# Kernel optimization log

Hardware: AMD Instinct MI355X
Metric: run time of the kernel (lower is better)

## Reference

```python
import jax, jax.numpy as jnp
import numpy as np

EPS = 1e-6

def _phi(u):
    # positive feature map used by linear attention
    return jax.nn.elu(u) + 1.0

def setup_inputs() -> dict:
    key = jax.random.key(0)
    ks = jax.random.split(key, 5)
    B, T, D = 8, 2048, 512  # batch, seq_len, d_model == in_features == out_features
    scale = 1.0 / np.sqrt(D)
    x = jax.random.normal(ks[0], (B, T, D), dtype=jnp.float32)
    Wq = (jax.random.normal(ks[1], (D, D), dtype=jnp.float32) * scale)
    Wk = (jax.random.normal(ks[2], (D, D), dtype=jnp.float32) * scale)
    Wv = (jax.random.normal(ks[3], (D, D), dtype=jnp.float32) * scale)
    Wp = (jax.random.normal(ks[4], (D, D), dtype=jnp.float32) * scale)  # output projection (bias=False)
    return {"x": x, "Wq": Wq, "Wk": Wk, "Wv": Wv, "Wp": Wp}

def reference(x, Wq, Wk, Wv, Wp):
    # x: [B, T, D]
    B, T, D = x.shape
    q = _phi(x @ Wq)  # [B, T, D]
    k = _phi(x @ Wk)  # [B, T, D]
    v = x @ Wv        # [B, T, D]

    # recurrent linear-attention cell, stepped over time via lax.scan
    def step(carry, qkv):
        S, z = carry              # S: [B, D, D] running sum of k^T v; z: [B, D] running sum of k
        qt, kt, vt = qkv          # each [B, D]
        S = S + kt[:, :, None] * vt[:, None, :]
        z = z + kt
        num = jnp.einsum('bd,bde->be', qt, S)        # [B, D]
        den = jnp.einsum('bd,bd->b', qt, z) + EPS    # [B]
        return (S, z), num / den[:, None]

    qT = jnp.swapaxes(q, 0, 1)  # [T, B, D]
    kT = jnp.swapaxes(k, 0, 1)
    vT = jnp.swapaxes(v, 0, 1)
    init = (jnp.zeros((B, D, D), dtype=x.dtype), jnp.zeros((B, D), dtype=x.dtype))
    _, yT = jax.lax.scan(step, init, (qT, kT, vT))  # yT: [T, B, D]
    y = jnp.swapaxes(yT, 0, 1)                      # [B, T, D]
    return y @ Wp                                   # final bias-free projection
```

## Files before the change

### kernel.cpp

```cpp
#include <hip/hip_runtime.h>


typedef __attribute__((ext_vector_type(4))) float f32x4;
typedef __attribute__((ext_vector_type(8))) __bf16 bf16x8;
typedef __attribute__((ext_vector_type(8))) unsigned short ushort8;

constexpr size_t OFF_XB  = 0;
constexpr size_t OFF_WT  = OFF_XB + 16777216;
constexpr size_t OFF_Q   = OFF_WT + 2097152;
constexpr size_t OFF_KK  = OFF_Q  + 16777216;
constexpr size_t OFF_KT  = OFF_KK + 16777216;
constexpr size_t OFF_VT  = OFF_KT + 16777216;
constexpr size_t OFF_MT  = OFF_VT + 16777216;
constexpr size_t OFF_Y   = OFF_MT + 33554432;
constexpr size_t OFF_ZP  = OFF_Y  + 16777216;
constexpr size_t WS_NEED = OFF_ZP + 262144;

__device__ __forceinline__ unsigned short bfbits(float f) {
  __bf16 h = (__bf16)f;
  return __builtin_bit_cast(unsigned short, h);
}
__device__ __forceinline__ float bff(unsigned short u) {
  return (float)__builtin_bit_cast(__bf16, u);
}

__device__ __forceinline__ void gload16(const void* g, void* l) {
  __builtin_amdgcn_global_load_lds((const __attribute__((address_space(1))) void*)g,
                                   (__attribute__((address_space(3))) void*)l, 16, 0, 0);
}

__device__ __forceinline__ void stage_half(const char* gRow0, size_t ld2, int k0b,
                                           char* ldsHalf, int w, int lane) {
#pragma unroll
  for (int i = 0; i < 2; ++i) {
    int L = (w << 10) + (lane << 4) + (i << 13);
    int r = L >> 7;
    int cb = (L & 127) ^ ((r & 7) << 4);
    gload16(gRow0 + (size_t)r * ld2 + k0b + cb, ldsHalf + (w << 10) + (i << 13));
  }
}

__device__ __forceinline__ void stage_q64(const char* gRow0, size_t ld2, int k0b,
                                          char* lds, int tid) {
  int L = tid << 4;
  int r = L >> 7;
  int cb = (L & 127) ^ ((r & 7) << 4);
  gload16(gRow0 + (size_t)r * ld2 + k0b + cb, lds + L);
}

__device__ __forceinline__ const bf16x8* frag_at(const char* halfBase, int rowInHalf,
                                                 int colByte) {
  int lin = (rowInHalf << 7) + colByte;
  lin ^= (rowInHalf & 7) << 4;
  return (const bf16x8*)(halfBase + lin);
}

#define QUADH(mh, nh)                                                                  \
  _Pragma("unroll") for (int mm = 0; mm < 2; ++mm)                                     \
  _Pragma("unroll") for (int nn = 0; nn < 2; ++nn)                                     \
  _Pragma("unroll") for (int s = 0; s < 2; ++s)                                        \
      acc[(mh)*2 + mm][(nh)*2 + nn] = __builtin_amdgcn_mfma_f32_16x16x32_bf16(         \
          af[(mh)*2 + mm][s], bg[(nh)*2 + nn][s], acc[(mh)*2 + mm][(nh)*2 + nn], 0, 0, 0);

#define PHASE_TAILH(MH, NH)                                      \
  __builtin_amdgcn_s_barrier();                                  \
  asm volatile("s_waitcnt lgkmcnt(0)" ::: "memory");             \
  __builtin_amdgcn_sched_barrier(0);                             \
  __builtin_amdgcn_s_setprio(1);                                 \
  QUADH(MH, NH);                                                 \
  __builtin_amdgcn_s_setprio(0);                                 \
  __builtin_amdgcn_s_barrier();

__device__ __forceinline__ void core8h(const char* Ab, size_t lda2, const char* Bb,
                                       size_t ldb2, int nt, char* sA, char* sB,
                                       f32x4 (&acc)[4][4], int w, int lane) {
  const int wr = w >> 2, wc = w & 3;
  const int fr = lane & 15, foB = (lane >> 4) << 4;
  const int brow = (wc & 1) << 6;
  const char* gB1 = Bb + (size_t)128 * ldb2;
  bf16x8 af[4][2], bg[4][2];

  stage_half(Ab, lda2, 0, sA + 0, w, lane);
  stage_half(Bb, ldb2, 0, sB + 0, w, lane);
  stage_half(gB1, ldb2, 0, sB + 16384, w, lane);
  if (nt > 1) {
    stage_half(Ab, lda2, 128, sA + 16384, w, lane);
    asm volatile("s_waitcnt vmcnt(2)" ::: "memory");
  } else {
    asm volatile("s_waitcnt vmcnt(0)" ::: "memory");
  }
  __builtin_amdgcn_sched_barrier(0);
  __builtin_amdgcn_s_barrier();

  for (int t = 0; t < nt; ++t) {
    const int buf = t & 1;
    const char* cA = sA + buf * 16384;
    const char* cB = sB + buf * 32768 + (wc >> 1) * 16384;
    char* nA = sA + buf * 16384;
    char* nB = sB + (buf ^ 1) * 32768;
    const int kb1 = (t + 1) << 7, kb2 = (t + 2) << 7;
    const bool stB = (t + 1 < nt), stA = (t + 2 < nt);

#pragma unroll
    for (int m = 0; m < 2; ++m)
#pragma unroll
      for (int s = 0; s < 2; ++s)
        af[m][s] = *frag_at(cA, wr * 64 + m * 16 + fr, s * 64 + foB);
#pragma unroll
    for (int n = 0; n < 2; ++n)
#pragma unroll
      for (int s = 0; s < 2; ++s)
        bg[n][s] = *frag_at(cB, brow + n * 16 + fr, s * 64 + foB);
    if (stB) stage_half(Bb, ldb2, kb1, nB + 0, w, lane);
    PHASE_TAILH(0, 0)

#pragma unroll
    for (int m = 2; m < 4; ++m)
#pragma unroll
      for (int s = 0; s < 2; ++s)
        af[m][s] = *frag_at(cA, wr * 64 + m * 16 + fr, s * 64 + foB);
    if (stB) stage_half(gB1, ldb2, kb1, nB + 16384, w, lane);
    PHASE_TAILH(1, 0)

#pragma unroll
    for (int n = 2; n < 4; ++n)
#pragma unroll
      for (int s = 0; s < 2; ++s)
        bg[n][s] = *frag_at(cB, brow + n * 16 + fr, s * 64 + foB);
    if (stA) stage_half(Ab, lda2, kb2, nA, w, lane);
    PHASE_TAILH(0, 1)

    if (t < nt - 1) {
      if (stA) {
        asm volatile("s_waitcnt vmcnt(2)" ::: "memory");
      } else {
        asm volatile("s_waitcnt vmcnt(0)" ::: "memory");
      }
      __builtin_amdgcn_sched_barrier(0);
    }
    PHASE_TAILH(1, 1)
  }
}

__device__ __forceinline__ void core8h_ldsA(const char* sG, const char* Bb, size_t ldb2,
                                            int nt, char* sB, f32x4 (&acc)[4][4],
                                            int w, int lane) {
  const int wr = w >> 2, wc = w & 3;
  const int fr = lane & 15, foB = (lane >> 4) << 4;
  const int brow = (wc & 1) << 6;
  const char* gB1 = Bb + (size_t)128 * ldb2;
  bf16x8 af[4][2], bg[4][2];

  stage_half(Bb, ldb2, 0, sB + 0, w, lane);
  stage_half(gB1, ldb2, 0, sB + 16384, w, lane);
  asm volatile("s_waitcnt vmcnt(0)" ::: "memory");
  __builtin_amdgcn_sched_barrier(0);
  __builtin_amdgcn_s_barrier();

  for (int t = 0; t < nt; ++t) {
    const int buf = t & 1;
    const char* cA = sG + t * 16384;
    const char* cB = sB + buf * 32768 + (wc >> 1) * 16384;
    char* nB = sB + (buf ^ 1) * 32768;
    if (t + 1 < nt) {
      stage_half(Bb, ldb2, (t + 1) << 7, nB + 0, w, lane);
      stage_half(gB1, ldb2, (t + 1) << 7, nB + 16384, w, lane);
    }
#pragma unroll
    for (int m = 0; m < 4; ++m)
#pragma unroll
      for (int s = 0; s < 2; ++s)
        af[m][s] = *frag_at(cA, wr * 64 + m * 16 + fr, s * 64 + foB);
#pragma unroll
    for (int n = 0; n < 4; ++n)
#pragma unroll
      for (int s = 0; s < 2; ++s)
        bg[n][s] = *frag_at(cB, brow + n * 16 + fr, s * 64 + foB);
    __builtin_amdgcn_s_setprio(1);
#pragma unroll
    for (int m = 0; m < 4; ++m)
#pragma unroll
      for (int n = 0; n < 4; ++n)
#pragma unroll
        for (int s = 0; s < 2; ++s)
          acc[m][n] = __builtin_amdgcn_mfma_f32_16x16x32_bf16(af[m][s], bg[n][s],
                                                              acc[m][n], 0, 0, 0);
    __builtin_amdgcn_s_setprio(0);
    if (t + 1 < nt) {
      asm volatile("s_waitcnt vmcnt(0)" ::: "memory");
      __builtin_amdgcn_sched_barrier(0);
      __builtin_amdgcn_s_barrier();
    }
  }
}

#define ACC4_INIT                                    \
  f32x4 acc[4][4];                                   \
  _Pragma("unroll") for (int m_ = 0; m_ < 4; ++m_)   \
  _Pragma("unroll") for (int n_ = 0; n_ < 4; ++n_)   \
      acc[m_][n_] = f32x4{0.f, 0.f, 0.f, 0.f};

#define ACC4_ZERO                                    \
  _Pragma("unroll") for (int m_ = 0; m_ < 4; ++m_)   \
  _Pragma("unroll") for (int n_ = 0; n_ < 4; ++n_)   \
      acc[m_][n_] = f32x4{0.f, 0.f, 0.f, 0.f};

__global__ __launch_bounds__(512, 2) void k8_qkvt(const ushort* __restrict__ xb,
                                                  const ushort* __restrict__ wt,
                                                  ushort* __restrict__ qb,
                                                  ushort* __restrict__ kkb,
                                                  ushort* __restrict__ Kt,
                                                  ushort* __restrict__ Vt,
                                                  float* __restrict__ zsumH) {
  extern __shared__ char smem[];
  const int o = blockIdx.x;
  const int wg = (o & 7) * 64 + (o >> 3);
  const int mt = wg >> 2, ct = wg & 3;
  const int tid = threadIdx.x, w = tid >> 6, lane = tid & 63;
  const int wr = w >> 2, wc = w & 3;
  const int fr = lane & 15, foB = (lane >> 4) << 4, q4 = (lane >> 4) << 2;
  const char* Ab = (const char*)(xb + (size_t)mt * 128 * 512);
  const char* Bz[3];
  Bz[0] = (const char*)(wt + (size_t)ct * 65536);
  Bz[1] = (const char*)(wt + 262144 + (size_t)ct * 65536);
  Bz[2] = (const char*)(wt + 524288 + (size_t)ct * 65536);
  char* sA = smem;
  char* sB0 = smem + 32768;
  char* sB1 = smem + 65536;
  char* sB2 = smem + 98304;

  f32x4 acc[3][4][2];
#pragma unroll
  for (int z = 0; z < 3; ++z)
#pragma unroll
    for (int m = 0; m < 4; ++m)
#pragma unroll
      for (int n = 0; n < 2; ++n) acc[z][m][n] = f32x4{0.f, 0.f, 0.f, 0.f};

  stage_half(Ab, 1024, 0, sA, w, lane);
  stage_half(Bz[0], 1024, 0, sB0, w, lane);
  stage_half(Bz[1], 1024, 0, sB1, w, lane);
  stage_half(Bz[2], 1024, 0, sB2, w, lane);
  asm volatile("s_waitcnt vmcnt(0)" ::: "memory");
  __builtin_amdgcn_sched_barrier(0);
  __builtin_amdgcn_s_barrier();

  for (int t = 0; t < 8; ++t) {
    const int buf = t & 1;
    const int bo = buf << 14, nbo = (buf ^ 1) << 14;
    if (t + 1 < 8) {
      const int kb = (t + 1) << 7;
      stage_half(Ab, 1024, kb, sA + nbo, w, lane);
      stage_half(Bz[0], 1024, kb, sB0 + nbo, w, lane);
      stage_half(Bz[1], 1024, kb, sB1 + nbo, w, lane);
      stage_half(Bz[2], 1024, kb, sB2 + nbo, w, lane);
    }
    bf16x8 af[4][2], bg[3][2][2];
#pragma unroll
    for (int m = 0; m < 4; ++m)
#pragma unroll
      for (int s = 0; s < 2; ++s)
        af[m][s] = *frag_at(sA + bo, wr * 64 + m * 16 + fr, s * 64 + foB);
#pragma unroll
    for (int z = 0; z < 3; ++z)
#pragma unroll
      for (int n = 0; n < 2; ++n)
#pragma unroll
        for (int s = 0; s < 2; ++s)
          bg[z][n][s] = *frag_at((z == 0 ? sB0 : z == 1 ? sB1 : sB2) + bo,
                                 wc * 32 + n * 16 + fr, s * 64 + foB);
    __builtin_amdgcn_s_setprio(1);
#pragma unroll
    for (int z = 0; z < 3; ++z)
#pragma unroll
      for (int m = 0; m < 4; ++m)
#pragma unroll
        for (int n = 0; n < 2; ++n)
#pragma unroll
          for (int s = 0; s < 2; ++s)
            acc[z][m][n] = __builtin_amdgcn_mfma_f32_16x16x32_bf16(af[m][s], bg[z][n][s],
                                                                   acc[z][m][n], 0, 0, 0);
    __builtin_amdgcn_s_setprio(0);
    if (t + 1 < 8) {
      asm volatile("s_waitcnt vmcnt(0)" ::: "memory");
    }
    __builtin_amdgcn_sched_barrier(0);
    __builtin_amdgcn_s_barrier();
  }

  const size_t row0 = (size_t)mt * 128 + wr * 64;
  const size_t col0 = (size_t)ct * 128 + wc * 32;
#pragma unroll
  for (int m = 0; m < 4; ++m)
#pragma unroll
    for (int n = 0; n < 2; ++n)
#pragma unroll
      for (int r = 0; r < 4; ++r) {
        float v = acc[0][m][n][r];
        v = v > 0.f ? v + 1.f : __expf(v);
        qb[(row0 + m * 16 + q4 + r) * 512 + col0 + n * 16 + fr] = bfbits(v);
      }
#pragma unroll
  for (int m = 0; m < 4; ++m)
#pragma unroll
    for (int n = 0; n < 2; ++n) {
      ushort4 ov;
      ov.x = bfbits(acc[2][m][n][0]);
      ov.y = bfbits(acc[2][m][n][1]);
      ov.z = bfbits(acc[2][m][n][2]);
      ov.w = bfbits(acc[2][m][n][3]);
      *(ushort4*)&Vt[(col0 + n * 16 + fr) * 16384 + row0 + m * 16 + q4] = ov;
    }
  float zs[2] = {0.f, 0.f};
#pragma unroll
  for (int m = 0; m < 4; ++m)
#pragma unroll
    for (int n = 0; n < 2; ++n) {
      float ph[4];
#pragma unroll
      for (int r = 0; r < 4; ++r) {
        float v = acc[1][m][n][r];
        ph[r] = v > 0.f ? v + 1.f : __expf(v);
        kkb[(row0 + m * 16 + q4 + r) * 512 + col0 + n * 16 + fr] = bfbits(ph[r]);
        zs[n] += ph[r];
      }
      ushort4 ov;
      ov.x = bfbits(ph[0]); ov.y = bfbits(ph[1]); ov.z = bfbits(ph[2]); ov.w = bfbits(ph[3]);
      *(ushort4*)&Kt[(col0 + n * 16 + fr) * 16384 + row0 + m * 16 + q4] = ov;
    }
#pragma unroll
  for (int n = 0; n < 2; ++n) {
    zs[n] += __shfl_xor(zs[n], 16, 64);
    zs[n] += __shfl_xor(zs[n], 32, 64);
  }
  float* zbuf = (float*)smem;
  if (lane < 16) {
#pragma unroll
    for (int n = 0; n < 2; ++n) zbuf[wr * 128 + wc * 32 + n * 16 + fr] = zs[n];
  }
  __syncthreads();
  if (tid < 128)
    zsumH[(size_t)mt * 512 + ct * 128 + tid] = zbuf[tid] + zbuf[128 + tid];
}

__global__ __launch_bounds__(512, 2) void k8_mtst(const ushort* __restrict__ Kt,
                                                  const ushort* __restrict__ Vt,
                                                  ushort* __restrict__ Mt) {
  __shared__ __align__(16) char smem[49152];
  const int o = blockIdx.x;
  const int b = o & 7, r8 = o >> 3;
  const int et = r8 >> 3, dt = r8 & 7;
  const int tid = threadIdx.x, w = tid >> 6, lane = tid & 63;
  const int wr = w >> 2, wc = w & 3, fr = lane & 15;
  const int foB = (lane >> 4) << 4, q4 = (lane >> 4) << 2;
  const char* Ab = (const char*)(Vt + (size_t)et * 128 * 16384 + b * 2048);
  const char* Bb = (const char*)(Kt + (size_t)dt * 64 * 16384 + b * 2048);
  f32x4 acc[4];
#pragma unroll
  for (int m = 0; m < 4; ++m) acc[m] = f32x4{0.f, 0.f, 0.f, 0.f};

  stage_half(Ab, 32768, 0, smem, w, lane);
  stage_q64(Bb, 32768, 0, smem + 32768, tid);
  asm volatile("s_waitcnt vmcnt(0)" ::: "memory");
  __builtin_amdgcn_sched_barrier(0);
  __builtin_amdgcn_s_barrier();

  const int colg = dt * 64 + wc * 16 + fr;
  for (int kk = 0; kk < 32; ++kk) {
    const int c = kk >> 2, buf = kk & 1;
    if ((kk & 3) == 0) {
      ushort* Sc = Mt + (size_t)(b * 8 + c) * 262144 + colg;
#pragma unroll
      for (int m = 0; m < 4; ++m)
#pragma unroll
        for (int r = 0; r < 4; ++r)
          Sc[(size_t)(et * 128 + wr * 64 + m * 16 + q4 + r) * 512] = bfbits(acc[m][r]);
    }
    if (kk + 1 < 32) {
      const int k0b = ((kk + 1) >> 2) * 512 + ((kk + 1) & 3) * 128;
      stage_half(Ab, 32768, k0b, smem + ((buf ^ 1) << 14), w, lane);
      stage_q64(Bb, 32768, k0b, smem + 32768 + ((buf ^ 1) << 13), tid);
    }
    const char* cA = smem + (buf << 14);
    const char* cB = smem + 32768 + (buf << 13);
    bf16x8 af[4][2], bg[2];
#pragma unroll
    for (int s = 0; s < 2; ++s) bg[s] = *frag_at(cB, wc * 16 + fr, s * 64 + foB);
#pragma unroll
    for (int m = 0; m < 4; ++m)
#pragma unroll
      for (int s = 0; s < 2; ++s)
        af[m][s] = *frag_at(cA, wr * 64 + m * 16 + fr, s * 64 + foB);
    __builtin_amdgcn_s_setprio(1);
#pragma unroll
    for (int m = 0; m < 4; ++m)
#pragma unroll
      for (int s = 0; s < 2; ++s)
        acc[m] = __builtin_amdgcn_mfma_f32_16x16x32_bf16(af[m][s], bg[s], acc[m], 0, 0, 0);
    __builtin_amdgcn_s_setprio(0);
    asm volatile("s_waitcnt vmcnt(0)" ::: "memory");
    __builtin_amdgcn_sched_barrier(0);
    __builtin_amdgcn_s_barrier();
  }
}

__global__ __launch_bounds__(512, 2) void k8_y(const ushort* __restrict__ qb,
                                               const ushort* __restrict__ kkb,
                                               const ushort* __restrict__ St,
                                               const ushort* __restrict__ Vt,
                                               const float* __restrict__ zsumH,
                                               ushort* __restrict__ Y) {
  extern __shared__ char smem[];
  const int o = blockIdx.x;
  const int wg = (o & 7) * 32 + (o >> 3);
  const int bc = wg >> 2, rh = (wg >> 1) & 1, ch = wg & 1;
  const int b = bc >> 3, c = bc & 7;
  const int tid = threadIdx.x, w = tid >> 6, lane = tid & 63;
  const int wr = w >> 2, wc = w & 3, fr = lane & 15, q4 = (lane >> 4) << 2;
  char* sA = smem + 65536;
  char* sB = smem + 98304;
  const char* qptr = (const char*)(qb + (size_t)bc * 131072 + (size_t)rh * 65536);

  ACC4_INIT
  core8h(qptr, 1024, (const char*)(kkb + (size_t)bc * 131072), 1024, 8, sA, sB, acc, w, lane);

  float rs[4][4];
#pragma unroll
  for (int m = 0; m < 4; ++m)
#pragma unroll
    for (int r = 0; r < 4; ++r) rs[m][r] = 0.f;
#pragma unroll
  for (int m = 0; m < 4; ++m)
#pragma unroll
    for (int n = 0; n < 4; ++n)
#pragma unroll
      for (int r = 0; r < 4; ++r) {
        int rowL = wr * 64 + m * 16 + q4 + r;
        int col = wc * 64 + n * 16 + fr;
        float v = (col <= rh * 128 + rowL) ? acc[m][n][r] : 0.f;
        rs[m][r] += v;
        int byte = (rowL << 7) + ((col & 63) << 1);
        byte ^= (rowL & 7) << 4;
        *(__bf16*)(smem + (wc << 14) + byte) = (__bf16)v;
      }
#pragma unroll
  for (int m = 0; m < 4; ++m)
#pragma unroll
    for (int r = 0; r < 4; ++r) {
      rs[m][r] += __shfl_xor(rs[m][r], 1, 64);
      rs[m][r] += __shfl_xor(rs[m][r], 2, 64);
      rs[m][r] += __shfl_xor(rs[m][r], 4, 64);
      rs[m][r] += __shfl_xor(rs[m][r], 8, 64);
    }
  float* red = (float*)sA;
  float* zpl = red + 512;
  float* dend = zpl + 512;
  if (fr == 0) {
#pragma unroll
    for (int m = 0; m < 4; ++m)
#pragma unroll
      for (int r = 0; r < 4; ++r) red[wc * 128 + wr * 64 + m * 16 + q4 + r] = rs[m][r];
  }
  {
    float a = 0.f;
    for (int cp = 0; cp < c; ++cp)
      a += zsumH[(size_t)((b * 8 + cp) * 2) * 512 + tid] +
           zsumH[(size_t)((b * 8 + cp) * 2 + 1) * 512 + tid];
    zpl[tid] = a;
  }
  __syncthreads();
  {
    int rl = tid >> 2, quarter = tid & 3;
    int trow = bc * 256 + rh * 128 + rl;
    const ushort* qrow = qb + (size_t)trow * 512 + quarter * 128;
    const float* zq = zpl + quarter * 128;
    float s = 0.f;
    for (int j = 0; j < 128; j += 8) {
      ushort8 qv = *(const ushort8*)&qrow[j];
#pragma unroll
      for (int u = 0; u < 8; ++u) s = fmaf(bff(qv[u]), zq[j + u], s);
    }
    s += __shfl_xor(s, 1, 64);
    s += __shfl_xor(s, 2, 64);
    if (quarter == 0)
      dend[rl] = s + red[rl] + red[128 + rl] + red[256 + rl] + red[384 + rl] + 1e-6f;
  }
  __syncthreads();
  float dinv[4][4];
#pragma unroll
  for (int m = 0; m < 4; ++m)
#pragma unroll
    for (int r = 0; r < 4; ++r) dinv[m][r] = 1.f / dend[wr * 64 + m * 16 + q4 + r];
  __syncthreads();

  ACC4_ZERO
  core8h(qptr, 1024, (const char*)(St + (size_t)bc * 262144 + (size_t)ch * 131072), 1024, 8,
         sA, sB, acc, w, lane);
  core8h_ldsA(smem, (const char*)(Vt + (size_t)ch * 256 * 16384 + (size_t)bc * 256), 32768,
              rh ? 4 : 2, sB, acc, w, lane);

#pragma unroll
  for (int m = 0; m < 4; ++m)
#pragma unroll
    for (int n = 0; n < 4; ++n)
#pragma unroll
      for (int r = 0; r < 4; ++r) {
        size_t row = (size_t)bc * 256 + rh * 128 + wr * 64 + m * 16 + q4 + r;
        size_t col = (size_t)ch * 256 + wc * 64 + n * 16 + fr;
        Y[row * 512 + col] = bfbits(acc[m][n][r] * dinv[m][r]);
      }
}

__global__ __launch_bounds__(512, 2) void k8_out(const ushort* __restrict__ Y,
                                                 const ushort* __restrict__ wt,
                                                 float* __restrict__ out) {
  extern __shared__ char smem[];
  const int o = blockIdx.x;
  const int wg = (o & 7) * 32 + (o >> 3);
  const int mt = wg >> 1, ct = wg & 1;
  const int tid = threadIdx.x, w = tid >> 6, lane = tid & 63;
  ACC4_INIT
  core8h((const char*)(Y + (size_t)mt * 65536), 1024,
         (const char*)(wt + 786432 + (size_t)ct * 131072), 1024, 8,
         smem, smem + 32768, acc, w, lane);
  const int wr = w >> 2, wc = w & 3, fr = lane & 15, q4 = (lane >> 4) << 2;
  const size_t row0 = (size_t)mt * 128 + wr * 64;
  const size_t col0 = (size_t)ct * 256 + wc * 64;
#pragma unroll
  for (int m = 0; m < 4; ++m)
#pragma unroll
    for (int n = 0; n < 4; ++n)
#pragma unroll
      for (int r = 0; r < 4; ++r)
        out[(row0 + m * 16 + q4 + r) * 512 + col0 + n * 16 + fr] = acc[m][n][r];
}

__global__ __launch_bounds__(256) void k_pre(const float* __restrict__ x,
                                             const float* __restrict__ Wq,
                                             const float* __restrict__ Wk,
                                             const float* __restrict__ Wv,
                                             const float* __restrict__ Wp,
                                             ushort* __restrict__ xb,
                                             ushort* __restrict__ wt) {
  __shared__ float tile[64][65];
  if (blockIdx.x < 4096) {
    size_t i = ((size_t)blockIdx.x * 256 + threadIdx.x) * 8;
    float4 f0 = *(const float4*)&x[i], f1 = *(const float4*)&x[i + 4];
    ushort8 ov;
    ov[0] = bfbits(f0.x); ov[1] = bfbits(f0.y); ov[2] = bfbits(f0.z); ov[3] = bfbits(f0.w);
    ov[4] = bfbits(f1.x); ov[5] = bfbits(f1.y); ov[6] = bfbits(f1.z); ov[7] = bfbits(f1.w);
    *(ushort8*)&xb[i] = ov;
  } else {
    const int g = blockIdx.x - 4096;
    const int bz = g >> 6, rem = g & 63, bxw = rem >> 3, byw = rem & 7;
    const float* src = bz == 0 ? Wq : bz == 1 ? Wk : bz == 2 ? Wv : Wp;
    ushort* dst = wt + (size_t)bz * 262144;
    const int d0 = bxw * 64, n0 = byw * 64;
    const int tr = threadIdx.x >> 4, tc = (threadIdx.x & 15) << 2;
#pragma unroll
    for (int it = 0; it < 4; ++it) {
      float4 f = *(const float4*)&src[(size_t)(d0 + it * 16 + tr) * 512 + n0 + tc];
      tile[it * 16 + tr][tc + 0] = f.x;
      tile[it * 16 + tr][tc + 1] = f.y;
      tile[it * 16 + tr][tc + 2] = f.z;
      tile[it * 16 + tr][tc + 3] = f.w;
    }
    __syncthreads();
#pragma unroll
    for (int it = 0; it < 4; ++it) {
      int n = it * 16 + tr;
      ushort4 ov;
      ov.x = bfbits(tile[tc + 0][n]);
      ov.y = bfbits(tile[tc + 1][n]);
      ov.z = bfbits(tile[tc + 2][n]);
      ov.w = bfbits(tile[tc + 3][n]);
      *(ushort4*)&dst[(size_t)(n0 + n) * 512 + d0 + tc] = ov;
    }
  }
}

extern "C" void kernel_launch(void* const* d_in, const int* in_sizes, int n_in,
                              void* d_out, int out_size, void* d_ws, size_t ws_size,
                              hipStream_t stream) {
  const float* x  = (const float*)d_in[0];
  const float* Wq = (const float*)d_in[1];
  const float* Wk = (const float*)d_in[2];
  const float* Wv = (const float*)d_in[3];
  const float* Wp = (const float*)d_in[4];
  float* out = (float*)d_out;
  char* ws8 = (char*)d_ws;
  if (ws_size < WS_NEED) return;

  ushort* xb  = (ushort*)(ws8 + OFF_XB);
  ushort* wt  = (ushort*)(ws8 + OFF_WT);
  ushort* qb  = (ushort*)(ws8 + OFF_Q);
  ushort* kkb = (ushort*)(ws8 + OFF_KK);
  ushort* Kt  = (ushort*)(ws8 + OFF_KT);
  ushort* Vt  = (ushort*)(ws8 + OFF_VT);
  ushort* Mt  = (ushort*)(ws8 + OFF_MT);
  ushort* Y   = (ushort*)(ws8 + OFF_Y);
  float*  zpH = (float*)(ws8 + OFF_ZP);

  constexpr int SMEM_QKVT = 131072, SMEM_H = 98304, SMEM_Y = 163840;
  hipFuncSetAttribute((const void*)k8_qkvt, hipFuncAttributeMaxDynamicSharedMemorySize, SMEM_QKVT);
  hipFuncSetAttribute((const void*)k8_y,    hipFuncAttributeMaxDynamicSharedMemorySize, SMEM_Y);
  hipFuncSetAttribute((const void*)k8_out,  hipFuncAttributeMaxDynamicSharedMemorySize, SMEM_H);

  k_pre<<<4352, 256, 0, stream>>>(x, Wq, Wk, Wv, Wp, xb, wt);
  k8_qkvt<<<512, 512, SMEM_QKVT, stream>>>(xb, wt, qb, kkb, Kt, Vt, zpH);
  k8_mtst<<<256, 512, 0, stream>>>(Kt, Vt, Mt);
  k8_y<<<256, 512, SMEM_Y, stream>>>(qb, kkb, Mt, Vt, zpH, Y);
  k8_out<<<256, 512, SMEM_H, stream>>>(Y, wt, out);
}
```

Before: 127.2 us.

## Move intra-chunk QK^T gram and denominator into the state kernel

The masked intra-chunk score matrix (q·kᵀ), its row sums and the normalizing denominator move out of the output kernel. They are now computed by extra blocks added to the chunk-state kernel, so both pieces of work run concurrently across 384 blocks. The masked scores go to a global bf16 buffer and the denominators to a float buffer. The output kernel then streams the scores from global memory through the generic GEMM core, which cuts its LDS use from 160KB to 96KB and shortens its critical path. The cost is an extra global round trip for the score matrix, about 8MB, plus the extra workspace.

After: 127.6 us. About the same (+0.3%).

```diff
diff --git a/kernel.cpp b/kernel.cpp
--- a/kernel.cpp
+++ b/kernel.cpp
@@ -11,10 +11,12 @@
 constexpr size_t OFF_KK  = OFF_Q  + 16777216;
 constexpr size_t OFF_KT  = OFF_KK + 16777216;
 constexpr size_t OFF_VT  = OFF_KT + 16777216;
-constexpr size_t OFF_MT  = OFF_VT + 16777216;
+constexpr size_t OFF_G   = OFF_VT + 16777216;
+constexpr size_t OFF_MT  = OFF_G  + 8388608;
 constexpr size_t OFF_Y   = OFF_MT + 33554432;
 constexpr size_t OFF_ZP  = OFF_Y  + 16777216;
-constexpr size_t WS_NEED = OFF_ZP + 262144;
+constexpr size_t OFF_DEN = OFF_ZP + 262144;
+constexpr size_t WS_NEED = OFF_DEN + 65536;
 
 __device__ __forceinline__ unsigned short bfbits(float f) {
   __bf16 h = (__bf16)f;
@@ -139,58 +141,6 @@
       __builtin_amdgcn_sched_barrier(0);
     }
     PHASE_TAILH(1, 1)
-  }
-}
-
-__device__ __forceinline__ void core8h_ldsA(const char* sG, const char* Bb, size_t ldb2,
-                                            int nt, char* sB, f32x4 (&acc)[4][4],
-                                            int w, int lane) {
-  const int wr = w >> 2, wc = w & 3;
-  const int fr = lane & 15, foB = (lane >> 4) << 4;
-  const int brow = (wc & 1) << 6;
-  const char* gB1 = Bb + (size_t)128 * ldb2;
-  bf16x8 af[4][2], bg[4][2];
-
-  stage_half(Bb, ldb2, 0, sB + 0, w, lane);
-  stage_half(gB1, ldb2, 0, sB + 16384, w, lane);
-  asm volatile("s_waitcnt vmcnt(0)" ::: "memory");
-  __builtin_amdgcn_sched_barrier(0);
-  __builtin_amdgcn_s_barrier();
-
-  for (int t = 0; t < nt; ++t) {
-    const int buf = t & 1;
-    const char* cA = sG + t * 16384;
-    const char* cB = sB + buf * 32768 + (wc >> 1) * 16384;
-    char* nB = sB + (buf ^ 1) * 32768;
-    if (t + 1 < nt) {
-      stage_half(Bb, ldb2, (t + 1) << 7, nB + 0, w, lane);
-      stage_half(gB1, ldb2, (t + 1) << 7, nB + 16384, w, lane);
-    }
-#pragma unroll
-    for (int m = 0; m < 4; ++m)
-#pragma unroll
-      for (int s = 0; s < 2; ++s)
-        af[m][s] = *frag_at(cA, wr * 64 + m * 16 + fr, s * 64 + foB);
-#pragma unroll
-    for (int n = 0; n < 4; ++n)
-#pragma unroll
-      for (int s = 0; s < 2; ++s)
-        bg[n][s] = *frag_at(cB, brow + n * 16 + fr, s * 64 + foB);
-    __builtin_amdgcn_s_setprio(1);
-#pragma unroll
-    for (int m = 0; m < 4; ++m)
-#pragma unroll
-      for (int n = 0; n < 4; ++n)
-#pragma unroll
-        for (int s = 0; s < 2; ++s)
-          acc[m][n] = __builtin_amdgcn_mfma_f32_16x16x32_bf16(af[m][s], bg[n][s],
-                                                              acc[m][n], 0, 0, 0);
-    __builtin_amdgcn_s_setprio(0);
-    if (t + 1 < nt) {
-      asm volatile("s_waitcnt vmcnt(0)" ::: "memory");
-      __builtin_amdgcn_sched_barrier(0);
-      __builtin_amdgcn_s_barrier();
-    }
   }
 }
 
@@ -343,162 +293,171 @@
     zsumH[(size_t)mt * 512 + ct * 128 + tid] = zbuf[tid] + zbuf[128 + tid];
 }
 
-__global__ __launch_bounds__(512, 2) void k8_mtst(const ushort* __restrict__ Kt,
-                                                  const ushort* __restrict__ Vt,
-                                                  ushort* __restrict__ Mt) {
-  __shared__ __align__(16) char smem[49152];
-  const int o = blockIdx.x;
-  const int b = o & 7, r8 = o >> 3;
-  const int et = r8 >> 3, dt = r8 & 7;
+__global__ __launch_bounds__(512, 2) void k8_mg(const ushort* __restrict__ Kt,
+                                                const ushort* __restrict__ Vt,
+                                                const ushort* __restrict__ qb,
+                                                const ushort* __restrict__ kkb,
+                                                const float* __restrict__ zsumH,
+                                                ushort* __restrict__ Mt,
+                                                ushort* __restrict__ Gg,
+                                                float* __restrict__ den) {
+  extern __shared__ char smem[];
+  const int bx = blockIdx.x;
   const int tid = threadIdx.x, w = tid >> 6, lane = tid & 63;
   const int wr = w >> 2, wc = w & 3, fr = lane & 15;
   const int foB = (lane >> 4) << 4, q4 = (lane >> 4) << 2;
-  const char* Ab = (const char*)(Vt + (size_t)et * 128 * 16384 + b * 2048);
-  const char* Bb = (const char*)(Kt + (size_t)dt * 64 * 16384 + b * 2048);
-  f32x4 acc[4];
-#pragma unroll
-  for (int m = 0; m < 4; ++m) acc[m] = f32x4{0.f, 0.f, 0.f, 0.f};
-
-  stage_half(Ab, 32768, 0, smem, w, lane);
-  stage_q64(Bb, 32768, 0, smem + 32768, tid);
-  asm volatile("s_waitcnt vmcnt(0)" ::: "memory");
-  __builtin_amdgcn_sched_barrier(0);
-  __builtin_amdgcn_s_barrier();
-
-  const int colg = dt * 64 + wc * 16 + fr;
-  for (int kk = 0; kk < 32; ++kk) {
-    const int c = kk >> 2, buf = kk & 1;
-    if ((kk & 3) == 0) {
-      ushort* Sc = Mt + (size_t)(b * 8 + c) * 262144 + colg;
-#pragma unroll
-      for (int m = 0; m < 4; ++m)
-#pragma unroll
-        for (int r = 0; r < 4; ++r)
-          Sc[(size_t)(et * 128 + wr * 64 + m * 16 + q4 + r) * 512] = bfbits(acc[m][r]);
-    }
-    if (kk + 1 < 32) {
-      const int k0b = ((kk + 1) >> 2) * 512 + ((kk + 1) & 3) * 128;
-      stage_half(Ab, 32768, k0b, smem + ((buf ^ 1) << 14), w, lane);
-      stage_q64(Bb, 32768, k0b, smem + 32768 + ((buf ^ 1) << 13), tid);
-    }
-    const char* cA = smem + (buf << 14);
-    const char* cB = smem + 32768 + (buf << 13);
-    bf16x8 af[4][2], bg[2];
-#pragma unroll
-    for (int s = 0; s < 2; ++s) bg[s] = *frag_at(cB, wc * 16 + fr, s * 64 + foB);
-#pragma unroll
-    for (int m = 0; m < 4; ++m)
-#pragma unroll
-      for (int s = 0; s < 2; ++s)
-        af[m][s] = *frag_at(cA, wr * 64 + m * 16 + fr, s * 64 + foB);
-    __builtin_amdgcn_s_setprio(1);
-#pragma unroll
-    for (int m = 0; m < 4; ++m)
-#pragma unroll
-      for (int s = 0; s < 2; ++s)
-        acc[m] = __builtin_amdgcn_mfma_f32_16x16x32_bf16(af[m][s], bg[s], acc[m], 0, 0, 0);
-    __builtin_amdgcn_s_setprio(0);
+  if (bx < 256) {
+    const int b = bx & 7, r8 = bx >> 3;
+    const int et = r8 >> 3, dt = r8 & 7;
+    const char* Ab = (const char*)(Vt + (size_t)et * 128 * 16384 + b * 2048);
+    const char* Bb = (const char*)(Kt + (size_t)dt * 64 * 16384 + b * 2048);
+    f32x4 acc[4];
+#pragma unroll
+    for (int m = 0; m < 4; ++m) acc[m] = f32x4{0.f, 0.f, 0.f, 0.f};
+
+    stage_half(Ab, 32768, 0, smem, w, lane);
+    stage_q64(Bb, 32768, 0, smem + 32768, tid);
     asm volatile("s_waitcnt vmcnt(0)" ::: "memory");
     __builtin_amdgcn_sched_barrier(0);
     __builtin_amdgcn_s_barrier();
+
+    const int colg = dt * 64 + wc * 16 + fr;
+    for (int kk = 0; kk < 32; ++kk) {
+      const int c = kk >> 2, buf = kk & 1;
+      if ((kk & 3) == 0) {
+        ushort* Sc = Mt + (size_t)(b * 8 + c) * 262144 + colg;
+#pragma unroll
+        for (int m = 0; m < 4; ++m)
+#pragma unroll
+          for (int r = 0; r < 4; ++r)
+            Sc[(size_t)(et * 128 + wr * 64 + m * 16 + q4 + r) * 512] = bfbits(acc[m][r]);
+      }
+      if (kk + 1 < 32) {
+        const int k0b = ((kk + 1) >> 2) * 512 + ((kk + 1) & 3) * 128;
+        stage_half(Ab, 32768, k0b, smem + ((buf ^ 1) << 14), w, lane);
+        stage_q64(Bb, 32768, k0b, smem + 32768 + ((buf ^ 1) << 13), tid);
+      }
+      const char* cA = smem + (buf << 14);
+      const char* cB = smem + 32768 + (buf << 13);
+      bf16x8 af[4][2], bg[2];
+#pragma unroll
+      for (int s = 0; s < 2; ++s) bg[s] = *frag_at(cB, wc * 16 + fr, s * 64 + foB);
+#pragma unroll
+      for (int m = 0; m < 4; ++m)
+#pragma unroll
+        for (int s = 0; s < 2; ++s)
+          af[m][s] = *frag_at(cA, wr * 64 + m * 16 + fr, s * 64 + foB);
+      __builtin_amdgcn_s_setprio(1);
+#pragma unroll
+      for (int m = 0; m < 4; ++m)
+#pragma unroll
+        for (int s = 0; s < 2; ++s)
+          acc[m] = __builtin_amdgcn_mfma_f32_16x16x32_bf16(af[m][s], bg[s], acc[m], 0, 0, 0);
+      __builtin_amdgcn_s_setprio(0);
+      asm volatile("s_waitcnt vmcnt(0)" ::: "memory");
+      __builtin_amdgcn_sched_barrier(0);
+      __builtin_amdgcn_s_barrier();
+    }
+  } else {
+    const int g = bx - 256;
+    const int bc = g >> 1, rh = g & 1;
+    const int b = bc >> 3, c = bc & 7;
+    char* sA = smem;
+    char* sB = smem + 32768;
+    ACC4_INIT
+    core8h((const char*)(qb + (size_t)bc * 131072 + (size_t)rh * 65536), 1024,
+           (const char*)(kkb + (size_t)bc * 131072), 1024, 8, sA, sB, acc, w, lane);
+
+    float rs[4][4];
+#pragma unroll
+    for (int m = 0; m < 4; ++m)
+#pragma unroll
+      for (int r = 0; r < 4; ++r) rs[m][r] = 0.f;
+#pragma unroll
+    for (int m = 0; m < 4; ++m)
+#pragma unroll
+      for (int n = 0; n < 4; ++n)
+#pragma unroll
+        for (int r = 0; r < 4; ++r) {
+          int rowL = wr * 64 + m * 16 + q4 + r;
+          int col = wc * 64 + n * 16 + fr;
+          float v = (col <= rh * 128 + rowL) ? acc[m][n][r] : 0.f;
+          rs[m][r] += v;
+          Gg[(size_t)bc * 65536 + (size_t)(rh * 128 + rowL) * 256 + col] = bfbits(v);
+        }
+#pragma unroll
+    for (int m = 0; m < 4; ++m)
+#pragma unroll
+      for (int r = 0; r < 4; ++r) {
+        rs[m][r] += __shfl_xor(rs[m][r], 1, 64);
+        rs[m][r] += __shfl_xor(rs[m][r], 2, 64);
+        rs[m][r] += __shfl_xor(rs[m][r], 4, 64);
+        rs[m][r] += __shfl_xor(rs[m][r], 8, 64);
+      }
+    float* red = (float*)sA;
+    float* zpl = red + 512;
+    if (fr == 0) {
+#pragma unroll
+      for (int m = 0; m < 4; ++m)
+#pragma unroll
+        for (int r = 0; r < 4; ++r) red[wc * 128 + wr * 64 + m * 16 + q4 + r] = rs[m][r];
+    }
+    {
+      float a = 0.f;
+      for (int cp = 0; cp < c; ++cp)
+        a += zsumH[(size_t)((b * 8 + cp) * 2) * 512 + tid] +
+             zsumH[(size_t)((b * 8 + cp) * 2 + 1) * 512 + tid];
+      zpl[tid] = a;
+    }
+    __syncthreads();
+    {
+      int rl = tid >> 2, quarter = tid & 3;
+      int trow = bc * 256 + rh * 128 + rl;
+      const ushort* qrow = qb + (size_t)trow * 512 + quarter * 128;
+      const float* zq = zpl + quarter * 128;
+      float s = 0.f;
+      for (int j = 0; j < 128; j += 8) {
+        ushort8 qv = *(const ushort8*)&qrow[j];
+#pragma unroll
+        for (int u = 0; u < 8; ++u) s = fmaf(bff(qv[u]), zq[j + u], s);
+      }
+      s += __shfl_xor(s, 1, 64);
+      s += __shfl_xor(s, 2, 64);
+      if (quarter == 0)
+        den[trow] = s + red[rl] + red[128 + rl] + red[256 + rl] + red[384 + rl] + 1e-6f;
+    }
   }
 }
 
 __global__ __launch_bounds__(512, 2) void k8_y(const ushort* __restrict__ qb,
-                                               const ushort* __restrict__ kkb,
+                                               const ushort* __restrict__ Gg,
                                                const ushort* __restrict__ St,
                                                const ushort* __restrict__ Vt,
-                                               const float* __restrict__ zsumH,
+                                               const float* __restrict__ den,
                                                ushort* __restrict__ Y) {
   extern __shared__ char smem[];
   const int o = blockIdx.x;
   const int wg = (o & 7) * 32 + (o >> 3);
   const int bc = wg >> 2, rh = (wg >> 1) & 1, ch = wg & 1;
-  const int b = bc >> 3, c = bc & 7;
   const int tid = threadIdx.x, w = tid >> 6, lane = tid & 63;
   const int wr = w >> 2, wc = w & 3, fr = lane & 15, q4 = (lane >> 4) << 2;
-  char* sA = smem + 65536;
-  char* sB = smem + 98304;
-  const char* qptr = (const char*)(qb + (size_t)bc * 131072 + (size_t)rh * 65536);
+  char* sA = smem;
+  char* sB = smem + 32768;
 
   ACC4_INIT
-  core8h(qptr, 1024, (const char*)(kkb + (size_t)bc * 131072), 1024, 8, sA, sB, acc, w, lane);
-
-  float rs[4][4];
+  core8h((const char*)(qb + (size_t)bc * 131072 + (size_t)rh * 65536), 1024,
+         (const char*)(St + (size_t)bc * 262144 + (size_t)ch * 131072), 1024, 8,
+         sA, sB, acc, w, lane);
+  core8h((const char*)(Gg + (size_t)bc * 65536 + (size_t)rh * 32768), 512,
+         (const char*)(Vt + (size_t)ch * 256 * 16384 + (size_t)bc * 256), 32768,
+         rh ? 4 : 2, sA, sB, acc, w, lane);
+
+  float dinv[4][4];
 #pragma unroll
   for (int m = 0; m < 4; ++m)
 #pragma unroll
-    for (int r = 0; r < 4; ++r) rs[m][r] = 0.f;
-#pragma unroll
-  for (int m = 0; m < 4; ++m)
-#pragma unroll
-    for (int n = 0; n < 4; ++n)
-#pragma unroll
-      for (int r = 0; r < 4; ++r) {
-        int rowL = wr * 64 + m * 16 + q4 + r;
-        int col = wc * 64 + n * 16 + fr;
-        float v = (col <= rh * 128 + rowL) ? acc[m][n][r] : 0.f;
-        rs[m][r] += v;
-        int byte = (rowL << 7) + ((col & 63) << 1);
-        byte ^= (rowL & 7) << 4;
-        *(__bf16*)(smem + (wc << 14) + byte) = (__bf16)v;
-      }
-#pragma unroll
-  for (int m = 0; m < 4; ++m)
-#pragma unroll
-    for (int r = 0; r < 4; ++r) {
-      rs[m][r] += __shfl_xor(rs[m][r], 1, 64);
-      rs[m][r] += __shfl_xor(rs[m][r], 2, 64);
-      rs[m][r] += __shfl_xor(rs[m][r], 4, 64);
-      rs[m][r] += __shfl_xor(rs[m][r], 8, 64);
-    }
-  float* red = (float*)sA;
-  float* zpl = red + 512;
-  float* dend = zpl + 512;
-  if (fr == 0) {
-#pragma unroll
-    for (int m = 0; m < 4; ++m)
-#pragma unroll
-      for (int r = 0; r < 4; ++r) red[wc * 128 + wr * 64 + m * 16 + q4 + r] = rs[m][r];
-  }
-  {
-    float a = 0.f;
-    for (int cp = 0; cp < c; ++cp)
-      a += zsumH[(size_t)((b * 8 + cp) * 2) * 512 + tid] +
-           zsumH[(size_t)((b * 8 + cp) * 2 + 1) * 512 + tid];
-    zpl[tid] = a;
-  }
-  __syncthreads();
-  {
-    int rl = tid >> 2, quarter = tid & 3;
-    int trow = bc * 256 + rh * 128 + rl;
-    const ushort* qrow = qb + (size_t)trow * 512 + quarter * 128;
-    const float* zq = zpl + quarter * 128;
-    float s = 0.f;
-    for (int j = 0; j < 128; j += 8) {
-      ushort8 qv = *(const ushort8*)&qrow[j];
-#pragma unroll
-      for (int u = 0; u < 8; ++u) s = fmaf(bff(qv[u]), zq[j + u], s);
-    }
-    s += __shfl_xor(s, 1, 64);
-    s += __shfl_xor(s, 2, 64);
-    if (quarter == 0)
-      dend[rl] = s + red[rl] + red[128 + rl] + red[256 + rl] + red[384 + rl] + 1e-6f;
-  }
-  __syncthreads();
-  float dinv[4][4];
-#pragma unroll
-  for (int m = 0; m < 4; ++m)
-#pragma unroll
-    for (int r = 0; r < 4; ++r) dinv[m][r] = 1.f / dend[wr * 64 + m * 16 + q4 + r];
-  __syncthreads();
-
-  ACC4_ZERO
-  core8h(qptr, 1024, (const char*)(St + (size_t)bc * 262144 + (size_t)ch * 131072), 1024, 8,
-         sA, sB, acc, w, lane);
-  core8h_ldsA(smem, (const char*)(Vt + (size_t)ch * 256 * 16384 + (size_t)bc * 256), 32768,
-              rh ? 4 : 2, sB, acc, w, lane);
-
+    for (int r = 0; r < 4; ++r)
+      dinv[m][r] = 1.f / den[bc * 256 + rh * 128 + wr * 64 + m * 16 + q4 + r];
 #pragma unroll
   for (int m = 0; m < 4; ++m)
 #pragma unroll
@@ -597,18 +556,21 @@
   ushort* kkb = (ushort*)(ws8 + OFF_KK);
   ushort* Kt  = (ushort*)(ws8 + OFF_KT);
   ushort* Vt  = (ushort*)(ws8 + OFF_VT);
+  ushort* Gg  = (ushort*)(ws8 + OFF_G);
   ushort* Mt  = (ushort*)(ws8 + OFF_MT);
   ushort* Y   = (ushort*)(ws8 + OFF_Y);
   float*  zpH = (float*)(ws8 + OFF_ZP);
-
-  constexpr int SMEM_QKVT = 131072, SMEM_H = 98304, SMEM_Y = 163840;
+  float*  den = (float*)(ws8 + OFF_DEN);
+
+  constexpr int SMEM_QKVT = 131072, SMEM_H = 98304;
   hipFuncSetAttribute((const void*)k8_qkvt, hipFuncAttributeMaxDynamicSharedMemorySize, SMEM_QKVT);
-  hipFuncSetAttribute((const void*)k8_y,    hipFuncAttributeMaxDynamicSharedMemorySize, SMEM_Y);
+  hipFuncSetAttribute((const void*)k8_mg,   hipFuncAttributeMaxDynamicSharedMemorySize, SMEM_H);
+  hipFuncSetAttribute((const void*)k8_y,    hipFuncAttributeMaxDynamicSharedMemorySize, SMEM_H);
   hipFuncSetAttribute((const void*)k8_out,  hipFuncAttributeMaxDynamicSharedMemorySize, SMEM_H);
 
   k_pre<<<4352, 256, 0, stream>>>(x, Wq, Wk, Wv, Wp, xb, wt);
   k8_qkvt<<<512, 512, SMEM_QKVT, stream>>>(xb, wt, qb, kkb, Kt, Vt, zpH);
-  k8_mtst<<<256, 512, 0, stream>>>(Kt, Vt, Mt);
-  k8_y<<<256, 512, SMEM_Y, stream>>>(qb, kkb, Mt, Vt, zpH, Y);
+  k8_mg<<<384, 512, SMEM_H, stream>>>(Kt, Vt, qb, kkb, zpH, Mt, Gg, den);
+  k8_y<<<256, 512, SMEM_H, stream>>>(qb, Gg, Mt, Vt, den, Y);
   k8_out<<<256, 512, SMEM_H, stream>>>(Y, wt, out);
 }
```
